# Performance work log

Hardware: AMD Instinct MI355X
Metric: run time of the kernel (lower is better)

The kernel has to match this reference:

```python
import jax, jax.numpy as jnp
import numpy as np

B, N, D, K = 4, 4096, 64, 16
SCALE = float(np.sqrt(D))


def setup_inputs() -> dict:
    key = jax.random.key(0)
    ks = jax.random.split(key, 16)
    f = lambda i, shape: jax.random.normal(ks[i], shape, dtype=jnp.float32) * 0.05
    return {
        'x': jax.random.normal(ks[0], (B, N, D), dtype=jnp.float32),
        'pos': jax.random.uniform(ks[1], (B, N, 3), dtype=jnp.float32),
        'Wq': f(2, (D, D)), 'Wk': f(3, (D, D)), 'Wv': f(4, (D, D)),
        'P1': f(5, (3, D)), 'p1b': f(6, (D,)), 'P2': f(7, (D, D)), 'p2b': f(8, (D,)),
        'A1': f(9, (D, D)), 'a1b': f(10, (D,)), 'A2': f(11, (D, D)), 'a2b': f(12, (D,)),
        'Wf': f(13, (D, D)), 'bf': f(14, (D,)),
    }


def _gather(feats, idx):
    # feats: [B,N,C], idx: [B,N,K] -> [B,N,K,C]  (index_points / idx_pt)
    return jax.vmap(lambda f, i: f[i])(feats, idx)


def reference(x, pos, Wq, Wk, Wv, P1, p1b, P2, p2b, A1, a1b, A2, a2b, Wf, bf):
    # kNN via squared distances (same math as square_distance + argsort[:, :, :k])
    sq = jnp.sum(pos * pos, axis=-1)                                   # [B,N]
    dists = sq[:, :, None] + sq[:, None, :] - 2.0 * jnp.einsum('bnc,bmc->bnm', pos, pos)
    _, idx = jax.lax.top_k(-dists, K)                                  # [B,N,K]

    knn_xyz = _gather(pos, idx)                                        # [B,N,K,3]
    q = x @ Wq                                                         # [B,N,D]
    kf = _gather(x @ Wk, idx)                                          # [B,N,K,D]
    v = _gather(x @ Wv, idx)                                           # [B,N,K,D]

    rel = pos[:, :, None, :] - knn_xyz                                 # [B,N,K,3]
    pos_enc = jax.nn.relu(rel @ P1 + p1b) @ P2 + p2b                   # [B,N,K,D]

    attn = jax.nn.relu((q[:, :, None, :] - kf + pos_enc) @ A1 + a1b) @ A2 + a2b
    attn = jax.nn.softmax(attn / SCALE, axis=-2)                       # softmax over K

    agg = jnp.sum(attn * (v + pos_enc), axis=2)                        # [B,N,D]
    return agg @ Wf + bf + x                                           # residual
```

## Files before the change

### kernel.cpp

```cpp
#include <hip/hip_runtime.h>
#include <hip/hip_bf16.h>
#include <stdint.h>

#define B_ 4
#define N_ 4096
#define D_ 64
#define K_ 16

static const size_t OFS_WQA1  = 0;
static const size_t OFS_WKA1  = 4096;
static const size_t OFS_WCOMB = 8192;
static const size_t OFS_C1    = 16384;
static const size_t OFS_QA1   = 16448;
static const size_t OFS_KA1   = OFS_QA1 + (size_t)B_*N_*64;
static const size_t OFS_V     = OFS_KA1 + (size_t)B_*N_*64;
static const size_t OFS_IDX   = OFS_V   + (size_t)B_*N_*64;
static const size_t OFS_POS4  = OFS_IDX + (size_t)B_*N_*16;
static const size_t OFS_BF16  = OFS_POS4 + (size_t)B_*N_*4;
static const size_t OFS_PBF   = OFS_BF16 + 6144;
static const size_t OFS_WFB   = OFS_PBF + 6144;

typedef __attribute__((ext_vector_type(8))) short short8;
typedef __attribute__((ext_vector_type(4))) float floatx4;

__device__ __forceinline__ unsigned short f2bf(float f) {
    __hip_bfloat16 h = __float2bfloat16(f);
    return *reinterpret_cast<unsigned short*>(&h);
}

__device__ __forceinline__ void bsortu64x2(unsigned long long& a, unsigned long long& b, int l) {
#pragma unroll
    for (int k = 2; k <= 64; k <<= 1) {
#pragma unroll
        for (int j = k >> 1; j > 0; j >>= 1) {
            unsigned long long oa = __shfl_xor(a, j, 64);
            unsigned long long ob = __shfl_xor(b, j, 64);
            bool up = (((l & j) == 0) == ((l & k) == 0));
            unsigned long long mna = a < oa ? a : oa, mxa = a < oa ? oa : a;
            unsigned long long mnb = b < ob ? b : ob, mxb = b < ob ? ob : b;
            a = up ? mna : mxa;
            b = up ? mnb : mxb;
        }
    }
}

__global__ __launch_bounds__(256) void k_pre(
        const float* __restrict__ Wq, const float* __restrict__ Wk,
        const float* __restrict__ Wv, const float* __restrict__ Wf,
        const float* __restrict__ P2, const float* __restrict__ A1,
        const float* __restrict__ p2b, const float* __restrict__ a1b,
        const float* __restrict__ pos, float* __restrict__ ws) {
    int blk = blockIdx.x;
    unsigned short* pbf = (unsigned short*)(ws + OFS_PBF);
    if (blk < 65) {
        int i = blk * 256 + threadIdx.x;
        if (i < 4096) {
            int c = i >> 6, d = i & 63;
            float s = 0.f;
            for (int e = 0; e < 64; ++e) s = fmaf(Wq[c*64+e], A1[e*64+d], s);
            ws[OFS_WQA1 + i] = s;
            pbf[d*64 + c] = f2bf(s);
        } else if (i < 8192) {
            int j = i - 4096; int c = j >> 6, d = j & 63;
            float s = 0.f;
            for (int e = 0; e < 64; ++e) s = fmaf(Wk[c*64+e], A1[e*64+d], s);
            ws[OFS_WKA1 + j] = s;
            pbf[(64+d)*64 + c] = f2bf(s);
        } else if (i < 16384) {
            int j = i - 8192; int c = j >> 7, dd = j & 127;
            float s;
            if (dd < 64) { s = 0.f; for (int e = 0; e < 64; ++e) s = fmaf(P2[c*64+e], A1[e*64+dd], s); }
            else s = P2[c*64 + (dd - 64)];
            ws[OFS_WCOMB + j] = s;
        } else if (i < 16448) {
            int d = i - 16384;
            float s = a1b[d];
            for (int e = 0; e < 64; ++e) s = fmaf(p2b[e], A1[e*64+d], s);
            ws[OFS_C1 + d] = s;
        }
    } else if (blk < 81) {
        int i = (blk - 65) * 256 + threadIdx.x;
        int c = i >> 6, d = i & 63;
        pbf[(128+d)*64 + c] = f2bf(Wv[c*64+d]);
    } else if (blk < 97) {
        int i = (blk - 81) * 256 + threadIdx.x;
        int c = i >> 6, d = i & 63;
        ((unsigned short*)(ws + OFS_WFB))[d*64 + c] = f2bf(Wf[c*64+d]);
    } else {
        int i = (blk - 97) * 256 + threadIdx.x;
        float px = pos[(size_t)i*3+0], py = pos[(size_t)i*3+1], pz = pos[(size_t)i*3+2];
        float sq = fmaf(pz, pz, fmaf(py, py, px*px));
        ((float4*)(ws + OFS_POS4))[i] = make_float4(px, py, pz, sq);
    }
}

__global__ __launch_bounds__(256) void k_projm(const float* __restrict__ x,
                                               const float* __restrict__ A2,
                                               float* __restrict__ ws) {
    __shared__ unsigned short xT[64*72];
    __shared__ unsigned short wTs[192*72];
    const int t = threadIdx.x;
    if (blockIdx.x >= 256) {
        int i = ((int)blockIdx.x - 256) * 256 + t;
        unsigned short* wbf = (unsigned short*)(ws + OFS_BF16);
        if (i < 8192) {
            int c = i >> 7, dd = i & 127;
            wbf[dd*64 + c] = f2bf(ws[OFS_WCOMB + i]);
        } else {
            int j = i - 8192; int e = j >> 6, d = j & 63;
            wbf[8192 + d*64 + e] = f2bf(A2[j]);
        }
        return;
    }
    const unsigned short* pbf = (const unsigned short*)(ws + OFS_PBF);
    const int g0 = (int)blockIdx.x * 64;

#pragma unroll
    for (int k = 0; k < 6; ++k) {
        int id  = t + 256*k;
        int row = id >> 3, cir = id & 7;
        uint4 vv = *(const uint4*)(pbf + row*64 + cir*8);
        *(uint4*)&wTs[row*72 + cir*8] = vv;
    }
    {
        int r = t >> 2, qd = t & 3;
        const float* src = x + (size_t)(g0 + r)*64 + qd*16;
        unsigned short hb[16];
#pragma unroll
        for (int u = 0; u < 16; ++u) hb[u] = f2bf(src[u]);
        *(uint4*)&xT[r*72 + qd*16]     = *(uint4*)&hb[0];
        *(uint4*)&xT[r*72 + qd*16 + 8] = *(uint4*)&hb[8];
    }
    __syncthreads();

    const int w = t >> 6, l = t & 63, lr = l & 15, q = l >> 4;
    floatx4 acc[12];
#pragma unroll
    for (int j = 0; j < 12; ++j) acc[j] = (floatx4){0.f, 0.f, 0.f, 0.f};
#pragma unroll
    for (int kb = 0; kb < 2; ++kb) {
        short8 a = *(const short8*)&xT[(16*w + lr)*72 + 32*kb + 8*q];
#pragma unroll
        for (int j = 0; j < 12; ++j) {
            short8 bfr = *(const short8*)&wTs[(16*j + lr)*72 + 32*kb + 8*q];
            acc[j] = __builtin_amdgcn_mfma_f32_16x16x32_bf16(a, bfr, acc[j], 0, 0, 0);
        }
    }
    float* qA1 = ws + OFS_QA1;
    float* kA1 = ws + OFS_KA1;
    float* vws = ws + OFS_V;
#pragma unroll
    for (int j = 0; j < 12; ++j) {
        int col = 16*j + lr;
        float* dst = (col < 64) ? qA1 : (col < 128 ? kA1 : vws);
        int c2 = col & 63;
#pragma unroll
        for (int r = 0; r < 4; ++r) {
            int grow = g0 + 16*w + 4*q + r;
            dst[(size_t)grow*64 + c2] = acc[j][r];
        }
    }
}

__global__ __launch_bounds__(512) void k_knn(float* __restrict__ ws) {
    __shared__ float4 tile[2048];
    __shared__ unsigned long long sbuf[8*128];
    const float4* pos4 = (const float4*)(ws + OFS_POS4);
    int* idx = (int*)(ws + OFS_IDX);
    const int t = threadIdx.x;
    const int l = t & 63, wv = t >> 6;
    const int b = (int)(blockIdx.x >> 8);
    const int q0 = ((int)(blockIdx.x & 255)) * 16 + 2*wv;
    const size_t g0r = (size_t)b * N_ + q0;
    const float4* pb = pos4 + (size_t)b * N_;

    float4 qa = pos4[g0r];
    float4 qb = pos4[g0r + 1];
    float d0[32], d1[32];
    float mn0 = 1e30f, mn1 = 1e30f;

#pragma unroll
    for (int i = 0; i < 4; ++i) tile[t + 512*i] = pb[t + 512*i];
    __syncthreads();
#pragma unroll 8
    for (int i = 0; i < 32; ++i) {
        float4 cd = tile[i*64 + l];
        float dotA = fmaf(qa.z, cd.z, fmaf(qa.y, cd.y, qa.x*cd.x));
        float dA = fmaxf(fmaf(-2.f, dotA, qa.w + cd.w), 0.f);
        float dotB = fmaf(qb.z, cd.z, fmaf(qb.y, cd.y, qb.x*cd.x));
        float dB = fmaxf(fmaf(-2.f, dotB, qb.w + cd.w), 0.f);
        d0[i] = dA; d1[i] = dB;
        mn0 = fminf(mn0, dA); mn1 = fminf(mn1, dB);
    }
    __syncthreads();
#pragma unroll
    for (int i = 0; i < 4; ++i) tile[t + 512*i] = pb[2048 + t + 512*i];
    __syncthreads();
#pragma unroll 8
    for (int i = 0; i < 32; ++i) {
        float4 cd = tile[i*64 + l];
        float dotA = fmaf(qa.z, cd.z, fmaf(qa.y, cd.y, qa.x*cd.x));
        mn0 = fminf(mn0, fmaxf(fmaf(-2.f, dotA, qa.w + cd.w), 0.f));
        float dotB = fmaf(qb.z, cd.z, fmaf(qb.y, cd.y, qb.x*cd.x));
        mn1 = fminf(mn1, fmaxf(fmaf(-2.f, dotB, qb.w + cd.w), 0.f));
    }

    float v0 = mn0, v1 = mn1;
#pragma unroll
    for (int k = 2; k <= 64; k <<= 1) {
#pragma unroll
        for (int j = k >> 1; j > 0; j >>= 1) {
            float o0 = __shfl_xor(v0, j, 64);
            float o1 = __shfl_xor(v1, j, 64);
            bool up = (((l & j) == 0) == ((l & k) == 0));
            v0 = up ? fminf(v0, o0) : fmaxf(v0, o0);
            v1 = up ? fminf(v1, o1) : fmaxf(v1, o1);
        }
    }
    float tau0 = __shfl(v0, 15, 64);
    float tau1 = __shfl(v1, 15, 64);

    unsigned long long* sb0 = sbuf + wv*128;
    unsigned long long* sb1 = sb0 + 64;
    const unsigned long long lmask = (1ull << l) - 1ull;
    int cnt0 = 0, cnt1 = 0;
#pragma unroll 8
    for (int i = 0; i < 32; ++i) {
        bool p0 = (d0[i] <= tau0);
        unsigned long long m0 = __ballot(p0);
        if (p0) {
            int pp = cnt0 + __popcll(m0 & lmask);
            if (pp < 64)
                sb0[pp] = ((unsigned long long)__float_as_uint(d0[i]) << 32) | (unsigned)(i*64 + l);
        }
        cnt0 += (int)__popcll(m0);
        bool p1 = (d1[i] <= tau1);
        unsigned long long m1 = __ballot(p1);
        if (p1) {
            int pp = cnt1 + __popcll(m1 & lmask);
            if (pp < 64)
                sb1[pp] = ((unsigned long long)__float_as_uint(d1[i]) << 32) | (unsigned)(i*64 + l);
        }
        cnt1 += (int)__popcll(m1);
    }
#pragma unroll 4
    for (int i = 0; i < 32; ++i) {
        float4 cd = tile[i*64 + l];
        float dotA = fmaf(qa.z, cd.z, fmaf(qa.y, cd.y, qa.x*cd.x));
        float dA = fmaxf(fmaf(-2.f, dotA, qa.w + cd.w), 0.f);
        float dotB = fmaf(qb.z, cd.z, fmaf(qb.y, cd.y, qb.x*cd.x));
        float dB = fmaxf(fmaf(-2.f, dotB, qb.w + cd.w), 0.f);
        bool p0 = (dA <= tau0);
        unsigned long long m0 = __ballot(p0);
        if (p0) {
            int pp = cnt0 + __popcll(m0 & lmask);
            if (pp < 64)
                sb0[pp] = ((unsigned long long)__float_as_uint(dA) << 32) | (unsigned)(2048 + i*64 + l);
        }
        cnt0 += (int)__popcll(m0);
        bool p1 = (dB <= tau1);
        unsigned long long m1 = __ballot(p1);
        if (p1) {
            int pp = cnt1 + __popcll(m1 & lmask);
            if (pp < 64)
                sb1[pp] = ((unsigned long long)__float_as_uint(dB) << 32) | (unsigned)(2048 + i*64 + l);
        }
        cnt1 += (int)__popcll(m1);
    }
    if (cnt0 > 64) cnt0 = 64;
    if (cnt1 > 64) cnt1 = 64;

    unsigned long long pk0 = (l < cnt0) ? sb0[l] : ~0ull;
    unsigned long long pk1 = (l < cnt1) ? sb1[l] : ~0ull;
    bsortu64x2(pk0, pk1, l);
    if (l < 16) {
        idx[g0r*16 + l]       = (int)(pk0 & 0xffffffffu);
        idx[(g0r + 1)*16 + l] = (int)(pk1 & 0xffffffffu);
    }
}

__global__ __launch_bounds__(256) void k_attn(
    const float* __restrict__ x, const float* __restrict__ pos,
    const float* __restrict__ P1, const float* __restrict__ p1b,
    const float* __restrict__ p2b, const float* __restrict__ a2b,
    const float* __restrict__ bff, const float* __restrict__ ws,
    float* __restrict__ out) {

    __shared__ unsigned short wT[128*72];
    __shared__ unsigned short abuf[128*72];
    __shared__ float relb[128*4];
    __shared__ int   mrow[128];

    const int t  = threadIdx.x;
    const int g0 = blockIdx.x * 8;
    const int b  = g0 >> 12;
    const float* qA1 = ws + OFS_QA1;
    const float* kA1 = ws + OFS_KA1;
    const float* vws = ws + OFS_V;
    const float* c1  = ws + OFS_C1;
    const int* idx = (const int*)(ws + OFS_IDX);
    const unsigned short* wbf = (const unsigned short*)(ws + OFS_BF16);
    const unsigned short* wfb = (const unsigned short*)(ws + OFS_WFB);

    const int w = t >> 6, l = t & 63, lr = l & 15, q = l >> 4;

    short8 a2frag[2][4];
    {
        const unsigned short* a2g = wbf + 8192;
#pragma unroll
        for (int kb = 0; kb < 2; ++kb)
#pragma unroll
            for (int j = 0; j < 4; ++j)
                a2frag[kb][j] = *(const short8*)&a2g[(16*j + lr)*64 + 32*kb + 8*q];
    }

#pragma unroll
    for (int k = 0; k < 4; ++k) {
        int id  = t + 256*k;
        int row = id >> 3, cir = id & 7;
        uint4 vv = *(const uint4*)(wbf + row*64 + cir*8);
        *(uint4*)&wT[row*72 + cir*8] = vv;
    }

    if (t < 128) {
        int p = t >> 4, k = t & 15;
        int ng = g0 + p;
        int m  = idx[(size_t)ng*16 + k];
        int mg = b * N_ + m;
        mrow[t] = mg;
        relb[t*4+0] = pos[(size_t)ng*3+0] - pos[(size_t)mg*3+0];
        relb[t*4+1] = pos[(size_t)ng*3+1] - pos[(size_t)mg*3+1];
        relb[t*4+2] = pos[(size_t)ng*3+2] - pos[(size_t)mg*3+2];
    }
    __syncthreads();

    float kpre[2][4][4];
    float qpre[2][4];
#pragma unroll
    for (int i = 0; i < 2; ++i) {
        int ng = g0 + 2*w + i;
#pragma unroll
        for (int j = 0; j < 4; ++j) {
            int col = 16*j + lr;
            qpre[i][j] = qA1[(size_t)ng*64 + col] + c1[col];
#pragma unroll
            for (int r = 0; r < 4; ++r) {
                int row = 32*w + 16*i + 4*q + r;
                kpre[i][j][r] = kA1[(size_t)mrow[row]*64 + col];
            }
        }
    }

    {
        int d = t & 63, r0 = t >> 6;
        float w0 = P1[d], w1 = P1[64+d], w2 = P1[128+d], bb = p1b[d];
#pragma unroll
        for (int jj = 0; jj < 32; ++jj) {
            int r = r0 + jj*4;
            float h = fmaf(relb[r*4+2], w2, fmaf(relb[r*4+1], w1, fmaf(relb[r*4+0], w0, bb)));
            abuf[r*72 + d] = f2bf(fmaxf(h, 0.f));
        }
    }
    __syncthreads();

    floatx4 acc1[2][8];
#pragma unroll
    for (int i = 0; i < 2; ++i)
#pragma unroll
        for (int j = 0; j < 8; ++j) acc1[i][j] = (floatx4){0.f, 0.f, 0.f, 0.f};
#pragma unroll
    for (int kb = 0; kb < 2; ++kb) {
        short8 a0 = *(const short8*)&abuf[(32*w      + lr)*72 + 32*kb + 8*q];
        short8 a1 = *(const short8*)&abuf[(32*w + 16 + lr)*72 + 32*kb + 8*q];
#pragma unroll
        for (int j = 0; j < 8; ++j) {
            short8 bfr = *(const short8*)&wT[(16*j + lr)*72 + 32*kb + 8*q];
            acc1[0][j] = __builtin_amdgcn_mfma_f32_16x16x32_bf16(a0, bfr, acc1[0][j], 0, 0, 0);
            acc1[1][j] = __builtin_amdgcn_mfma_f32_16x16x32_bf16(a1, bfr, acc1[1][j], 0, 0, 0);
        }
    }
    __syncthreads();

#pragma unroll
    for (int i = 0; i < 2; ++i) {
#pragma unroll
        for (int j = 0; j < 4; ++j) {
            int col = 16*j + lr;
            float qv = qpre[i][j];
#pragma unroll
            for (int r = 0; r < 4; ++r) {
                int row = 32*w + 16*i + 4*q + r;
                float t1 = acc1[i][j][r] + qv - kpre[i][j][r];
                abuf[row*72 + col] = f2bf(fmaxf(t1, 0.f));
            }
        }
    }

    float vpre[2][4][4];
#pragma unroll
    for (int i = 0; i < 2; ++i)
#pragma unroll
        for (int j = 0; j < 4; ++j) {
            int col = 16*j + lr;
#pragma unroll
            for (int r = 0; r < 4; ++r) {
                int row = 32*w + 16*i + 4*q + r;
                vpre[i][j][r] = vws[(size_t)mrow[row]*64 + col];
            }
        }
    short8 wffrag[2];
#pragma unroll
    for (int kb = 0; kb < 2; ++kb)
        wffrag[kb] = *(const short8*)&wfb[(16*w + lr)*64 + 32*kb + 8*q];
    __syncthreads();

    floatx4 acc2[2][4];
#pragma unroll
    for (int i = 0; i < 2; ++i)
#pragma unroll
        for (int j = 0; j < 4; ++j) acc2[i][j] = (floatx4){0.f, 0.f, 0.f, 0.f};
#pragma unroll
    for (int kb = 0; kb < 2; ++kb) {
        short8 a0 = *(const short8*)&abuf[(32*w      + lr)*72 + 32*kb + 8*q];
        short8 a1 = *(const short8*)&abuf[(32*w + 16 + lr)*72 + 32*kb + 8*q];
#pragma unroll
        for (int j = 0; j < 4; ++j) {
            acc2[0][j] = __builtin_amdgcn_mfma_f32_16x16x32_bf16(a0, a2frag[kb][j], acc2[0][j], 0, 0, 0);
            acc2[1][j] = __builtin_amdgcn_mfma_f32_16x16x32_bf16(a1, a2frag[kb][j], acc2[1][j], 0, 0, 0);
        }
    }
    __syncthreads();

#pragma unroll
    for (int i = 0; i < 2; ++i) {
#pragma unroll
        for (int j = 0; j < 4; ++j) {
            int col = 16*j + lr;
            float a2bv = a2b[col], p2bv = p2b[col];
            float L[4];
#pragma unroll
            for (int r = 0; r < 4; ++r) L[r] = acc2[i][j][r] + a2bv;
            float mx = fmaxf(fmaxf(L[0], L[1]), fmaxf(L[2], L[3]));
            mx = fmaxf(mx, __shfl_xor(mx, 16, 64));
            mx = fmaxf(mx, __shfl_xor(mx, 32, 64));
            float ssum = 0.f, part = 0.f;
#pragma unroll
            for (int r = 0; r < 4; ++r) {
                float e = __expf((L[r] - mx) * 0.125f);
                ssum += e;
                float wv = vpre[i][j][r] + (acc1[i][4+j][r] + p2bv);
                part = fmaf(e, wv, part);
            }
            ssum += __shfl_xor(ssum, 16, 64);
            ssum += __shfl_xor(ssum, 32, 64);
            part += __shfl_xor(part, 16, 64);
            part += __shfl_xor(part, 32, 64);
            float agg = part / ssum;
            if (q == 0) abuf[(2*w + i)*72 + col] = f2bf(agg);
        }
    }
    __syncthreads();

    {
        floatx4 accF = (floatx4){0.f, 0.f, 0.f, 0.f};
#pragma unroll
        for (int kb = 0; kb < 2; ++kb) {
            short8 afr = *(const short8*)&abuf[lr*72 + 32*kb + 8*q];
            accF = __builtin_amdgcn_mfma_f32_16x16x32_bf16(afr, wffrag[kb], accF, 0, 0, 0);
        }
        if (q < 2) {
            int col = 16*w + lr;
            float bv = bff[col];
#pragma unroll
            for (int r = 0; r < 4; ++r) {
                int g = g0 + 4*q + r;
                out[(size_t)g*64 + col] = accF[r] + bv + x[(size_t)g*64 + col];
            }
        }
    }
}

extern "C" void kernel_launch(void* const* d_in, const int* in_sizes, int n_in,
                              void* d_out, int out_size, void* d_ws, size_t ws_size,
                              hipStream_t stream) {
    const float* x   = (const float*)d_in[0];
    const float* pos = (const float*)d_in[1];
    const float* Wq  = (const float*)d_in[2];
    const float* Wk  = (const float*)d_in[3];
    const float* Wv  = (const float*)d_in[4];
    const float* P1  = (const float*)d_in[5];
    const float* p1b = (const float*)d_in[6];
    const float* P2  = (const float*)d_in[7];
    const float* p2b = (const float*)d_in[8];
    const float* A1  = (const float*)d_in[9];
    const float* a1b = (const float*)d_in[10];
    const float* A2  = (const float*)d_in[11];
    const float* a2b = (const float*)d_in[12];
    const float* Wf  = (const float*)d_in[13];
    const float* bf  = (const float*)d_in[14];
    float* out = (float*)d_out;
    float* ws  = (float*)d_ws;

    hipLaunchKernelGGL(k_pre,   dim3(161),  dim3(256), 0, stream,
                       Wq, Wk, Wv, Wf, P2, A1, p2b, a1b, pos, ws);
    hipLaunchKernelGGL(k_projm, dim3(304),  dim3(256), 0, stream, x, A2, ws);
    hipLaunchKernelGGL(k_knn,   dim3(1024), dim3(512), 0, stream, ws);
    hipLaunchKernelGGL(k_attn,  dim3(2048), dim3(256), 0, stream,
                       x, pos, P1, p1b, p2b, a2b, bf, ws, out);
}
```

Baseline: 171.0 us.

## Merge projection and kNN kernels into one launch, move weight conversion to pre

The bf16 conversion of WCOMB and A2 moves into k_pre, so the projection kernel no longer needs its extra conversion blocks. The projection GEMM and the kNN search are merged into a single 512-thread kernel that interleaves one projection block per four kNN blocks, with shared memory reused between the two roles. Projection work is re-split across 8 waves with 6 MFMA tiles each. This removes one kernel launch and its serialization gap and lets projection blocks fill CU slots alongside kNN blocks. The cost is that both roles now share one block size and one shared-memory footprint, which may change occupancy for the kNN part.

```diff
diff --git a/kernel.cpp b/kernel.cpp
--- a/kernel.cpp
+++ b/kernel.cpp
@@ -47,11 +47,13 @@
 __global__ __launch_bounds__(256) void k_pre(
         const float* __restrict__ Wq, const float* __restrict__ Wk,
         const float* __restrict__ Wv, const float* __restrict__ Wf,
+        const float* __restrict__ A2,
         const float* __restrict__ P2, const float* __restrict__ A1,
         const float* __restrict__ p2b, const float* __restrict__ a1b,
         const float* __restrict__ pos, float* __restrict__ ws) {
     int blk = blockIdx.x;
     unsigned short* pbf = (unsigned short*)(ws + OFS_PBF);
+    unsigned short* wbf = (unsigned short*)(ws + OFS_BF16);
     if (blk < 65) {
         int i = blk * 256 + threadIdx.x;
         if (i < 4096) {
@@ -72,6 +74,7 @@
             if (dd < 64) { s = 0.f; for (int e = 0; e < 64; ++e) s = fmaf(P2[c*64+e], A1[e*64+dd], s); }
             else s = P2[c*64 + (dd - 64)];
             ws[OFS_WCOMB + j] = s;
+            wbf[dd*64 + c] = f2bf(s);
         } else if (i < 16448) {
             int d = i - 16384;
             float s = a1b[d];
@@ -86,63 +89,56 @@
         int i = (blk - 81) * 256 + threadIdx.x;
         int c = i >> 6, d = i & 63;
         ((unsigned short*)(ws + OFS_WFB))[d*64 + c] = f2bf(Wf[c*64+d]);
+    } else if (blk < 113) {
+        int i = (blk - 97) * 256 + threadIdx.x;
+        int e = i >> 6, d = i & 63;
+        wbf[8192 + d*64 + e] = f2bf(A2[i]);
     } else {
-        int i = (blk - 97) * 256 + threadIdx.x;
+        int i = (blk - 113) * 256 + threadIdx.x;
         float px = pos[(size_t)i*3+0], py = pos[(size_t)i*3+1], pz = pos[(size_t)i*3+2];
         float sq = fmaf(pz, pz, fmaf(py, py, px*px));
         ((float4*)(ws + OFS_POS4))[i] = make_float4(px, py, pz, sq);
     }
 }
 
-__global__ __launch_bounds__(256) void k_projm(const float* __restrict__ x,
-                                               const float* __restrict__ A2,
-                                               float* __restrict__ ws) {
-    __shared__ unsigned short xT[64*72];
-    __shared__ unsigned short wTs[192*72];
+
+__device__ __forceinline__ void projm_body(int pb, const float* __restrict__ x,
+                                           float* __restrict__ ws, char* smem) {
+    unsigned short* xT  = (unsigned short*)smem;
+    unsigned short* wTs = (unsigned short*)(smem + 9216);
     const int t = threadIdx.x;
-    if (blockIdx.x >= 256) {
-        int i = ((int)blockIdx.x - 256) * 256 + t;
-        unsigned short* wbf = (unsigned short*)(ws + OFS_BF16);
-        if (i < 8192) {
-            int c = i >> 7, dd = i & 127;
-            wbf[dd*64 + c] = f2bf(ws[OFS_WCOMB + i]);
-        } else {
-            int j = i - 8192; int e = j >> 6, d = j & 63;
-            wbf[8192 + d*64 + e] = f2bf(A2[j]);
-        }
-        return;
-    }
     const unsigned short* pbf = (const unsigned short*)(ws + OFS_PBF);
-    const int g0 = (int)blockIdx.x * 64;
-
-#pragma unroll
-    for (int k = 0; k < 6; ++k) {
-        int id  = t + 256*k;
+    const int g0 = pb * 64;
+
+#pragma unroll
+    for (int k = 0; k < 3; ++k) {
+        int id  = t + 512*k;
         int row = id >> 3, cir = id & 7;
         uint4 vv = *(const uint4*)(pbf + row*64 + cir*8);
         *(uint4*)&wTs[row*72 + cir*8] = vv;
     }
     {
-        int r = t >> 2, qd = t & 3;
-        const float* src = x + (size_t)(g0 + r)*64 + qd*16;
-        unsigned short hb[16];
-#pragma unroll
-        for (int u = 0; u < 16; ++u) hb[u] = f2bf(src[u]);
-        *(uint4*)&xT[r*72 + qd*16]     = *(uint4*)&hb[0];
-        *(uint4*)&xT[r*72 + qd*16 + 8] = *(uint4*)&hb[8];
-    }
-    __syncthreads();
-
-    const int w = t >> 6, l = t & 63, lr = l & 15, q = l >> 4;
-    floatx4 acc[12];
-#pragma unroll
-    for (int j = 0; j < 12; ++j) acc[j] = (floatx4){0.f, 0.f, 0.f, 0.f};
+        int r = t >> 3, qd = t & 7;
+        const float* src = x + (size_t)(g0 + r)*64 + qd*8;
+        unsigned short hb[8];
+#pragma unroll
+        for (int u = 0; u < 8; ++u) hb[u] = f2bf(src[u]);
+        *(uint4*)&xT[r*72 + qd*8] = *(uint4*)&hb[0];
+    }
+    __syncthreads();
+
+    const int w8 = t >> 6, l = t & 63, lr = l & 15, q = l >> 4;
+    const int wm = w8 & 3;
+    const int jb = (w8 >> 2) * 6;
+    floatx4 acc[6];
+#pragma unroll
+    for (int j = 0; j < 6; ++j) acc[j] = (floatx4){0.f, 0.f, 0.f, 0.f};
 #pragma unroll
     for (int kb = 0; kb < 2; ++kb) {
-        short8 a = *(const short8*)&xT[(16*w + lr)*72 + 32*kb + 8*q];
-#pragma unroll
-        for (int j = 0; j < 12; ++j) {
-            short8 bfr = *(const short8*)&wTs[(16*j + lr)*72 + 32*kb + 8*q];
+        short8 a = *(const short8*)&xT[(16*wm + lr)*72 + 32*kb + 8*q];
+#pragma unroll
+        for (int j = 0; j < 6; ++j) {
+            short8 bfr = *(const short8*)&wTs[(16*(jb+j) + lr)*72 + 32*kb + 8*q];
             acc[j] = __builtin_amdgcn_mfma_f32_16x16x32_bf16(a, bfr, acc[j], 0, 0, 0);
         }
     }
@@ -150,27 +146,27 @@
     float* kA1 = ws + OFS_KA1;
     float* vws = ws + OFS_V;
 #pragma unroll
-    for (int j = 0; j < 12; ++j) {
-        int col = 16*j + lr;
+    for (int j = 0; j < 6; ++j) {
+        int col = 16*(jb+j) + lr;
         float* dst = (col < 64) ? qA1 : (col < 128 ? kA1 : vws);
         int c2 = col & 63;
 #pragma unroll
         for (int r = 0; r < 4; ++r) {
-            int grow = g0 + 16*w + 4*q + r;
+            int grow = g0 + 16*wm + 4*q + r;
             dst[(size_t)grow*64 + c2] = acc[j][r];
         }
     }
 }
 
-__global__ __launch_bounds__(512) void k_knn(float* __restrict__ ws) {
-    __shared__ float4 tile[2048];
-    __shared__ unsigned long long sbuf[8*128];
+__device__ __forceinline__ void knn_body(int kid, float* __restrict__ ws, char* smem) {
+    float4* tile = (float4*)smem;
+    unsigned long long* sbuf = (unsigned long long*)(smem + 32768);
     const float4* pos4 = (const float4*)(ws + OFS_POS4);
     int* idx = (int*)(ws + OFS_IDX);
     const int t = threadIdx.x;
     const int l = t & 63, wv = t >> 6;
-    const int b = (int)(blockIdx.x >> 8);
-    const int q0 = ((int)(blockIdx.x & 255)) * 16 + 2*wv;
+    const int b = kid >> 8;
+    const int q0 = (kid & 255) * 16 + 2*wv;
     const size_t g0r = (size_t)b * N_ + q0;
     const float4* pb = pos4 + (size_t)b * N_;
 
@@ -277,6 +273,15 @@
         idx[g0r*16 + l]       = (int)(pk0 & 0xffffffffu);
         idx[(g0r + 1)*16 + l] = (int)(pk1 & 0xffffffffu);
     }
+}
+
+__global__ __launch_bounds__(512) void k_mid(const float* __restrict__ x,
+                                             float* __restrict__ ws) {
+    __shared__ __align__(16) char smem[40960];
+    int blk = blockIdx.x;
+    int m5 = blk % 5;
+    if (m5 == 4) projm_body(blk / 5, x, ws, smem);
+    else         knn_body((blk / 5) * 4 + m5, ws, smem);
 }
 
 __global__ __launch_bounds__(256) void k_attn(
@@ -501,10 +506,9 @@
     float* out = (float*)d_out;
     float* ws  = (float*)d_ws;
 
-    hipLaunchKernelGGL(k_pre,   dim3(161),  dim3(256), 0, stream,
-                       Wq, Wk, Wv, Wf, P2, A1, p2b, a1b, pos, ws);
-    hipLaunchKernelGGL(k_projm, dim3(304),  dim3(256), 0, stream, x, A2, ws);
-    hipLaunchKernelGGL(k_knn,   dim3(1024), dim3(512), 0, stream, ws);
-    hipLaunchKernelGGL(k_attn,  dim3(2048), dim3(256), 0, stream,
+    hipLaunchKernelGGL(k_pre,  dim3(177),  dim3(256), 0, stream,
+                       Wq, Wk, Wv, Wf, A2, P2, A1, p2b, a1b, pos, ws);
+    hipLaunchKernelGGL(k_mid,  dim3(1280), dim3(512), 0, stream, x, ws);
+    hipLaunchKernelGGL(k_attn, dim3(2048), dim3(256), 0, stream,
                        x, pos, P1, p1b, p2b, a2b, bf, ws, out);
 }
```

Result: slower. 175.8 us (+2.8%).
